# Performance work log

Hardware: AMD Instinct MI355X
Metric: run time of the kernel (lower is better)

## Reference

```python
import jax, jax.numpy as jnp
import numpy as np

N = 50000      # nodes
E = 800000     # edges (avg degree 16)
F_IN = 128
# (d_in, d_out) for the 9 GCNConv layers with width=256, n_layers=3
DIMS = [(128, 128), (128, 192), (192, 256), (256, 256), (256, 256), (256, 256), (256, 192), (192, 128), (128, 1)]
# ReLU after every conv except loop conv i==n_layers-2 (conv idx 4) and the final conv
RELU = [True, True, True, True, False, True, True, True, False]


def setup_inputs() -> dict:
    key = jax.random.key(0)
    ks = jax.random.split(key, 2 + 2 * len(DIMS))
    inp = {
        "x": jax.random.normal(ks[0], (N, F_IN), dtype=jnp.float32),
        "edge_index": jax.random.randint(ks[1], (2, E), 0, N, dtype=jnp.int64),
    }
    for i, (din, dout) in enumerate(DIMS):
        # Glorot-ish init for weights, small random bias (GCNConv has bias=True)
        inp[f"W{i}"] = jax.random.normal(ks[2 + 2 * i], (din, dout), dtype=jnp.float32) / np.float32(np.sqrt(din))
        inp[f"b{i}"] = jax.random.normal(ks[3 + 2 * i], (dout,), dtype=jnp.float32) * 0.01
    return inp


def _gcn_stack(x, src_f, dst_f, norm, Ws, bs):
    h = x
    for i in range(len(Ws)):
        h = h @ Ws[i]                                  # [N, dout] dense transform first (dout <= din mostly)
        msg = h[src_f] * norm[:, None]                 # gather + edge-normalize  [E+N, dout]
        h = jax.ops.segment_sum(msg, dst_f, num_segments=N) + bs[i]
        if RELU[i]:
            h = jax.nn.relu(h)
        # Dropout layers are identity in eval/inference mode.
    return h


def reference(x, edge_index,
              W0, b0, W1, b1, W2, b2, W3, b3, W4, b4, W5, b5, W6, b6, W7, b7, W8, b8):
    src, dst = edge_index[0], edge_index[1]
    loop = jnp.arange(N, dtype=src.dtype)
    # GCNConv default: add self loops, symmetric normalization D^{-1/2}(A+I)D^{-1/2}
    src_f = jnp.concatenate([src, loop])
    dst_f = jnp.concatenate([dst, loop])
    deg = jax.ops.segment_sum(jnp.ones(E + N, dtype=x.dtype), dst_f, num_segments=N)
    dinv = jax.lax.rsqrt(jnp.maximum(deg, 1.0))        # deg >= 1 thanks to self loops
    norm = dinv[src_f] * dinv[dst_f]                   # per-edge coefficient [E+N]
    Ws = [W0, W1, W2, W3, W4, W5, W6, W7, W8]
    bs = [b0, b1, b2, b3, b4, b5, b6, b7, b8]
    return _gcn_stack(x, src_f, dst_f, norm, Ws, bs)   # [N, 1]
```

## Files before the change

kernel.cpp:

```cpp
#include <hip/hip_runtime.h>


#define TPB 256

using bf16x8 = __attribute__((ext_vector_type(8))) __bf16;
using f32x4  = __attribute__((ext_vector_type(4))) float;
using f32x2  = __attribute__((ext_vector_type(2))) float;

__device__ __forceinline__ unsigned bf16rne(float x) {
    unsigned u = __float_as_uint(x);
    return (u + 0x7fffu + ((u >> 16) & 1u)) >> 16;
}

__device__ __forceinline__ void stage16(const unsigned short* g, unsigned short* l) {
#if __has_builtin(__builtin_amdgcn_global_load_lds)
    __builtin_amdgcn_global_load_lds((const __attribute__((address_space(1))) void*)g,
                                     (__attribute__((address_space(3))) void*)l, 16, 0, 0);
#else
    *(uint4*)((char*)l + (threadIdx.x & 63) * 16) = *(const uint4*)g;
#endif
}


__global__ void zinit_kernel(int* cnt, int* fill, unsigned* edges2, int n, int ecap) {
    int i = blockIdx.x * blockDim.x + threadIdx.x;
    if (i < n) { cnt[i] = 0; fill[i] = 0; }
    if (i < ecap) edges2[i] = 0u;
}

__global__ void count_kernel(const int* __restrict__ dst, int* __restrict__ cnt, int E) {
    int e = blockIdx.x * blockDim.x + threadIdx.x;
    if (e < E) atomicAdd(&cnt[dst[e]], 1);
}

__global__ void dinv_kernel(const int* __restrict__ cnt, float* __restrict__ dinv, int n) {
    int i = blockIdx.x * blockDim.x + threadIdx.x;
    if (i < n) dinv[i] = rsqrtf((float)(cnt[i] + 1));
}


__global__ void blockhist_kernel(const int* __restrict__ cnt, int* __restrict__ localRank,
                                 int* __restrict__ hb, int n, int nb) {
    __shared__ int h[64];
    int t = threadIdx.x;
    if (t < 64) h[t] = 0;
    __syncthreads();
    int i = blockIdx.x * TPB + t;
    if (i < n) {
        int d = cnt[i]; if (d > 63) d = 63;
        localRank[i] = atomicAdd(&h[d], 1);
    }
    __syncthreads();
    if (t < 64) hb[t * nb + blockIdx.x] = h[t];
}

__global__ __launch_bounds__(256) void sortscan_kernel(int* __restrict__ hb, int nb) {
    __shared__ int sh[64 * 256];
    __shared__ int tot[64], base[64];
    int t = threadIdx.x;
    int total = 64 * nb;
    for (int i = t; i < total; i += 256) sh[i] = hb[i];
    __syncthreads();
    if (t < 64) {
        int run = 0;
        for (int b = 0; b < nb; b++) {
            int v = sh[t * nb + b];
            sh[t * nb + b] = run;
            run += v;
        }
        tot[t] = run;
    }
    __syncthreads();
    if (t == 0) {
        int acc = 0;
        for (int b = 0; b < 64; b++) { base[b] = acc; acc += tot[b]; }
    }
    __syncthreads();
    for (int i = t; i < total; i += 256) hb[i] = sh[i] + base[i / nb];
}

__global__ void scatter2_kernel(const int* __restrict__ cnt,
                                const int* __restrict__ localRank, const int* __restrict__ hb,
                                int* __restrict__ perm, int* __restrict__ pcnt,
                                int* __restrict__ iperm, int n, int nb) {
    int i = blockIdx.x * TPB + threadIdx.x;
    if (i >= n) return;
    int c = cnt[i];
    int d = c; if (d > 63) d = 63;
    int pos = hb[d * nb + blockIdx.x] + localRank[i];
    perm[pos] = i;
    pcnt[pos] = c;
    iperm[i] = pos;
}

__global__ void scanpad_kernel(const int* __restrict__ pcnt, int* __restrict__ prowp2,
                               int* __restrict__ bsums, int n) {
    __shared__ int sh[TPB];
    int t = threadIdx.x;
    int i = blockIdx.x * TPB + t;
    int v = (i < n) ? ((pcnt[i] + 1 + 7) & ~7) : 0;
    sh[t] = v;
    __syncthreads();
    for (int off = 1; off < TPB; off <<= 1) {
        int x = (t >= off) ? sh[t - off] : 0;
        __syncthreads();
        sh[t] += x;
        __syncthreads();
    }
    if (i < n) prowp2[i] = sh[t] - v;
    if (t == TPB - 1) bsums[blockIdx.x] = sh[t];
}

__global__ void scan2_kernel(int* __restrict__ bsums, int nb) {
    __shared__ int sh[TPB];
    int t = threadIdx.x;
    int v = (t < nb) ? bsums[t] : 0;
    sh[t] = v;
    __syncthreads();
    for (int off = 1; off < TPB; off <<= 1) {
        int x = (t >= off) ? sh[t - off] : 0;
        __syncthreads();
        sh[t] += x;
        __syncthreads();
    }
    if (t < nb) bsums[t] = sh[t] - v;
}

__global__ void scan3_kernel(int* __restrict__ rowp, const int* __restrict__ bsums, int n) {
    int i = blockIdx.x * TPB + threadIdx.x;
    if (i < n) rowp[i] += bsums[blockIdx.x];
}

__global__ void fillself_kernel(const int* __restrict__ src, const int* __restrict__ dst,
                                const float* __restrict__ dinv,
                                const int* __restrict__ iperm, const int* __restrict__ prowp2,
                                int* __restrict__ fill, const int* __restrict__ cnt,
                                unsigned* __restrict__ edges2, int E, int n) {
    int id = blockIdx.x * blockDim.x + threadIdx.x;
    if (id < E) {
        int s = src[id], d = dst[id];
        int pos = prowp2[iperm[d]] + atomicAdd(&fill[d], 1);
        edges2[pos] = (unsigned)s | (bf16rne(dinv[s] * dinv[d]) << 16);
    } else if (id < E + n) {
        int i = id - E;
        float dv = dinv[i];
        edges2[prowp2[iperm[i]] + cnt[i]] = (unsigned)i | (bf16rne(dv * dv) << 16);
    }
}


struct WPtrs { const float* p[8]; };

__global__ void wt_all_kernel(WPtrs wp, unsigned short* __restrict__ Wts) {
    const int cum[9] = {0, 16384, 40960, 90112, 155648, 221184, 286720, 335872, 360448};
    const int Ns[8] = {128, 192, 256, 256, 256, 256, 192, 128};
    const int Ks[8] = {128, 128, 192, 256, 256, 256, 256, 192};
    int id = blockIdx.x * blockDim.x + threadIdx.x;
    if (id >= 360448) return;
    int L = 0;
#pragma unroll
    for (int t = 1; t < 8; t++) if (id >= cum[t]) L = t;
    int lid = id - cum[L];
    int N = Ns[L], K = Ks[L];
    int k = lid / N, n = lid - k * N;
    Wts[cum[L] + n * K + k] = (unsigned short)bf16rne(wp.p[L][lid]);
}

__global__ void cvt_bf16_kernel(const float* __restrict__ in, unsigned short* __restrict__ out,
                                int n4) {
    int i = blockIdx.x * blockDim.x + threadIdx.x;
    if (i >= n4) return;
    float4 v = ((const float4*)in)[i];
    uint2 o;
    o.x = bf16rne(v.x) | (bf16rne(v.y) << 16);
    o.y = bf16rne(v.z) | (bf16rne(v.w) << 16);
    ((uint2*)out)[i] = o;
}


__global__ __launch_bounds__(256) void gemm_mfma_kernel(
    const unsigned short* __restrict__ A, const unsigned short* __restrict__ Wt,
    const float* __restrict__ bias, unsigned short* __restrict__ C,
    int M, int K, int Nc, int doBias, int doRelu, int outChunked) {
    __shared__ unsigned short Qb[128 * 64];
    __shared__ unsigned short Pb[128 * 64];
    int tid = threadIdx.x;
    int l = tid & 63, w = tid >> 6;
    int node0 = blockIdx.x * 128, feat0 = blockIdx.y * 128;

    f32x4 acc[4][4];
#pragma unroll
    for (int i = 0; i < 4; i++)
#pragma unroll
        for (int j = 0; j < 4; j++) acc[i][j] = (f32x4){0.f, 0.f, 0.f, 0.f};

    const unsigned short* gQ[4];
    const unsigned short* gP[4];
    unsigned short* lQ[4];
    unsigned short* lP[4];
#pragma unroll
    for (int h = 0; h < 4; h++) {
        int slot = tid + h * 256;
        int r = slot >> 3, q = slot & 7;
        int qg = q ^ (r & 7);
        int nd = node0 + r; if (nd > M - 1) nd = M - 1;
        int ft = feat0 + r; if (ft > Nc - 1) ft = Nc - 1;
        gQ[h] = A + (size_t)nd * K + qg * 8;
        gP[h] = Wt + (size_t)ft * K + qg * 8;
        lQ[h] = Qb + (size_t)(w * 64 + h * 256) * 8;
        lP[h] = Pb + (size_t)(w * 64 + h * 256) * 8;
    }

    int q4 = l >> 4, m16 = l & 15;
    int featHalf = w & 1, nodeHalf = w >> 1;
    int rP0 = featHalf * 64 + m16;
    int rQ0 = nodeHalf * 64 + m16;
    int sw = m16 & 7;

    for (int k0 = 0; k0 < K; k0 += 64) {
        __syncthreads();
#pragma unroll
        for (int h = 0; h < 4; h++) {
            stage16(gQ[h] + k0, lQ[h]);
            stage16(gP[h] + k0, lP[h]);
        }
        __syncthreads();
#pragma unroll
        for (int ko = 0; ko < 2; ko++) {
            bf16x8 pf[4], qf[4];
#pragma unroll
            for (int i = 0; i < 4; i++)
                pf[i] = *(const bf16x8*)(Pb + (rP0 + i * 16) * 64 + ((ko * 4 + q4) ^ sw) * 8);
#pragma unroll
            for (int j = 0; j < 4; j++)
                qf[j] = *(const bf16x8*)(Qb + (rQ0 + j * 16) * 64 + ((ko * 4 + q4) ^ sw) * 8);
#pragma unroll
            for (int i = 0; i < 4; i++)
#pragma unroll
                for (int j = 0; j < 4; j++)
                    acc[i][j] = __builtin_amdgcn_mfma_f32_16x16x32_bf16(pf[i], qf[j],
                                                                        acc[i][j], 0, 0, 0);
        }
    }

#pragma unroll
    for (int i = 0; i < 4; i++) {
        int gf0 = feat0 + featHalf * 64 + i * 16 + q4 * 4;
        if (gf0 >= Nc) continue;
        float4 bv = make_float4(0.f, 0.f, 0.f, 0.f);
        if (doBias) bv = *(const float4*)(bias + gf0);
        size_t cb = outChunked ? ((size_t)(gf0 >> 5) * ((size_t)M * 32) + (gf0 & 31))
                               : (size_t)gf0;
#pragma unroll
        for (int j = 0; j < 4; j++) {
            int gn = node0 + nodeHalf * 64 + j * 16 + m16;
            if (gn >= M) continue;
            f32x4 v = acc[i][j];
            float x0 = v[0] + bv.x, x1 = v[1] + bv.y;
            float x2 = v[2] + bv.z, x3 = v[3] + bv.w;
            if (doRelu) {
                x0 = fmaxf(x0, 0.f); x1 = fmaxf(x1, 0.f);
                x2 = fmaxf(x2, 0.f); x3 = fmaxf(x3, 0.f);
            }
            uint2 o;
            o.x = bf16rne(x0) | (bf16rne(x1) << 16);
            o.y = bf16rne(x2) | (bf16rne(x3) << 16);
            size_t off = outChunked ? (cb + (size_t)gn * 32) : (cb + (size_t)gn * Nc);
            *(uint2*)(C + off) = o;
        }
    }
}

__global__ void gemv128_bf16_kernel(const unsigned short* __restrict__ A,
                                    const float* __restrict__ w,
                                    float* __restrict__ out, int M) {
    int wid = (blockIdx.x * blockDim.x + threadIdx.x) >> 6;
    int lane = threadIdx.x & 63;
    if (wid >= M) return;
    const unsigned short* a = A + (size_t)wid * 128;
    float a0 = __uint_as_float((unsigned)a[lane] << 16);
    float a1 = __uint_as_float((unsigned)a[lane + 64] << 16);
    float s = a0 * w[lane] + a1 * w[lane + 64];
#pragma unroll
    for (int off = 32; off > 0; off >>= 1) s += __shfl_down(s, off);
    if (lane == 0) out[wid] = s;
}


__global__ __launch_bounds__(256) void agg_group_kernel(
    const uint2* __restrict__ in, const int* __restrict__ prowp2,
    const int* __restrict__ pcnt, const int* __restrict__ perm,
    const unsigned* __restrict__ edges2,
    const float* __restrict__ bias, uint2* __restrict__ out,
    int Q, int upx, int ngPerUnit, int NG, int n_nodes, int rowVec2,
    int doBias, int doRelu, int outChunked) {
    int xcd = blockIdx.x & 7;
    int slot = blockIdx.x >> 3;
    int u = slot / ngPerUnit;
    int ngIdx = slot - u * ngPerUnit;
    int unit = xcd * upx + u;
    int chunk = unit / Q;
    int q = unit - chunk * Q;
    int ng = ngIdx * Q + q;
    if (ng >= NG) return;

    int wave = threadIdx.x >> 6;
    int lane = threadIdx.x & 63;
    int group = lane >> 3, fl = lane & 7;
    int i = ng * 32 + wave * 8 + group;
    if (i >= n_nodes) return;

    const uint2* sfl = in + (size_t)chunk * n_nodes * 8 + fl;
    int s0 = prowp2[i];
    int c = pcnt[i] + 1;
    int cpad = (c + 7) & ~7;
    int node = perm[i];
    const uint4* ep = (const uint4*)(edges2 + s0);

    f32x2 aA[4], aB[4];
#pragma unroll
    for (int k = 0; k < 4; k++) { aA[k] = (f32x2){0.f, 0.f}; aB[k] = (f32x2){0.f, 0.f}; }

    uint4 ea = ep[0], eb = ep[1];
    for (int base = 0; base < cpad; base += 8) {
        uint4 na = ep[2], nb = ep[3];
        ep += 2;
        unsigned e[8] = {ea.x, ea.y, ea.z, ea.w, eb.x, eb.y, eb.z, eb.w};
        uint2 p[8];
#pragma unroll
        for (int j = 0; j < 8; j++) p[j] = sfl[(size_t)(e[j] & 0xffffu) * 8];
#pragma unroll
        for (int j = 0; j < 8; j++) {
            float wgt = __uint_as_float(e[j] & 0xffff0000u);
            int k = j & 3;
            f32x2 v0 = {__uint_as_float(p[j].x << 16),
                        __uint_as_float(p[j].x & 0xffff0000u)};
            f32x2 v1 = {__uint_as_float(p[j].y << 16),
                        __uint_as_float(p[j].y & 0xffff0000u)};
            f32x2 w2 = {wgt, wgt};
            aA[k] += w2 * v0;
            aB[k] += w2 * v1;
        }
        ea = na; eb = nb;
    }
    f32x2 sA = (aA[0] + aA[1]) + (aA[2] + aA[3]);
    f32x2 sB = (aB[0] + aB[1]) + (aB[2] + aB[3]);

    if (doBias) {
        float4 bb = ((const float4*)bias)[chunk * 8 + fl];
        sA += (f32x2){bb.x, bb.y};
        sB += (f32x2){bb.z, bb.w};
    }
    if (doRelu) {
        sA[0] = fmaxf(sA[0], 0.f); sA[1] = fmaxf(sA[1], 0.f);
        sB[0] = fmaxf(sB[0], 0.f); sB[1] = fmaxf(sB[1], 0.f);
    }
    uint2 o;
    o.x = bf16rne(sA[0]) | (bf16rne(sA[1]) << 16);
    o.y = bf16rne(sB[0]) | (bf16rne(sB[1]) << 16);
    size_t oi = outChunked ? ((size_t)chunk * n_nodes * 8 + (size_t)node * 8 + fl)
                           : ((size_t)node * rowVec2 + chunk * 8 + fl);
    out[oi] = o;
}

__global__ void agg1_kernel(const float* __restrict__ in, const int* __restrict__ prowp2,
                            const int* __restrict__ pcnt, const int* __restrict__ perm,
                            const unsigned* __restrict__ edges2,
                            const float* __restrict__ bias, float* __restrict__ out,
                            int n_nodes) {
    int n = blockIdx.x * blockDim.x + threadIdx.x;
    if (n >= n_nodes) return;
    float acc = 0.f;
    int s0 = prowp2[n];
    int c = pcnt[n] + 1;
    for (int j = 0; j < c; j++) {
        unsigned e = edges2[s0 + j];
        acc += __uint_as_float(e & 0xffff0000u) * in[e & 0xffffu];
    }
    acc += bias[0];
    out[perm[n]] = acc;
}


extern "C" void kernel_launch(void* const* d_in, const int* in_sizes, int n_in,
                              void* d_out, int out_size, void* d_ws, size_t ws_size,
                              hipStream_t stream) {
    const float* x = (const float*)d_in[0];
    const int* ei = (const int*)d_in[1];
    const int Nn = in_sizes[0] / 128;
    const int E = in_sizes[1] / 2;
    const int* src = ei;
    const int* dst = ei + E;
    const int ecap = E + 8 * Nn + 64;

    char* ws = (char*)d_ws;
    size_t off = 0;
    auto alloc = [&](size_t bytes) -> char* {
        char* p = ws + off;
        off = (off + bytes + 255) & ~(size_t)255;
        return p;
    };
    int* cnt = (int*)alloc((size_t)Nn * 4);
    int* fill = (int*)alloc((size_t)Nn * 4);
    int* bsums = (int*)alloc(1024);
    float* dinv = (float*)alloc((size_t)Nn * 4);
    int* localRank = (int*)alloc((size_t)Nn * 4);
    int* hb = (int*)alloc((size_t)64 * 256 * 4);
    int* perm = (int*)alloc((size_t)Nn * 4);
    int* pcnt = (int*)alloc((size_t)Nn * 4);
    int* iperm = (int*)alloc((size_t)Nn * 4);
    int* prowp2 = (int*)alloc((size_t)Nn * 4);
    unsigned* edges2 = (unsigned*)alloc((size_t)ecap * 4);
    unsigned short* T = (unsigned short*)alloc((size_t)Nn * 256 * 2);
    unsigned short* H = (unsigned short*)alloc((size_t)Nn * 256 * 2);
    unsigned short* Bx = (unsigned short*)alloc((size_t)Nn * 128 * 2);
    float* F = (float*)alloc((size_t)Nn * 4);
    unsigned short* Wts = (unsigned short*)alloc((size_t)400000 * 2);
    (void)ws_size;

    const int dims[9][2] = {{128,128},{128,192},{192,256},{256,256},{256,256},
                            {256,256},{256,192},{192,128},{128,1}};
    unsigned short* Wt[8];
    {
        size_t o = 0;
        for (int i = 0; i < 8; i++) { Wt[i] = Wts + o; o += (size_t)dims[i][0] * dims[i][1]; }
    }

    int nbN = (Nn + TPB - 1) / TPB;
    int nbE = (E + TPB - 1) / TPB;
    int nbEN = (E + Nn + TPB - 1) / TPB;
    int nbC = (ecap + TPB - 1) / TPB;

    zinit_kernel<<<nbC, TPB, 0, stream>>>(cnt, fill, edges2, Nn, ecap);
    count_kernel<<<nbE, TPB, 0, stream>>>(dst, cnt, E);
    dinv_kernel<<<nbN, TPB, 0, stream>>>(cnt, dinv, Nn);
    blockhist_kernel<<<nbN, TPB, 0, stream>>>(cnt, localRank, hb, Nn, nbN);
    sortscan_kernel<<<1, 256, 0, stream>>>(hb, nbN);
    scatter2_kernel<<<nbN, TPB, 0, stream>>>(cnt, localRank, hb, perm, pcnt, iperm,
                                             Nn, nbN);
    scanpad_kernel<<<nbN, TPB, 0, stream>>>(pcnt, prowp2, bsums, Nn);
    scan2_kernel<<<1, TPB, 0, stream>>>(bsums, nbN);
    scan3_kernel<<<nbN, TPB, 0, stream>>>(prowp2, bsums, Nn);
    fillself_kernel<<<nbEN, TPB, 0, stream>>>(src, dst, dinv, iperm, prowp2, fill, cnt,
                                              edges2, E, Nn);

    WPtrs wp;
    for (int i = 0; i < 8; i++) wp.p[i] = (const float*)d_in[2 + 2 * i];
    wt_all_kernel<<<(360448 + TPB - 1) / TPB, TPB, 0, stream>>>(wp, Wts);
    cvt_bf16_kernel<<<(Nn * 32 + TPB - 1) / TPB, TPB, 0, stream>>>(x, Bx, Nn * 32);

    auto gemm = [&](const unsigned short* A, int i, unsigned short* C, int K, int Nc,
                    int doBias, int doRelu, int outChunked) {
        const float* b = (const float*)d_in[3 + 2 * i];
        dim3 grid((Nn + 127) / 128, (Nc + 127) / 128);
        gemm_mfma_kernel<<<grid, 256, 0, stream>>>(A, Wt[i], b, C, Nn, K, Nc,
                                                   doBias, doRelu, outChunked);
    };
    int NG = (Nn + 31) / 32;
    auto agg = [&](const unsigned short* inb, unsigned short* outb, int w, int i,
                   int doBias, int doRelu, int outChunked) {
        int nch = w / 32;
        int Q = (nch == 8) ? 1 : (nch == 6) ? 4 : 2;
        int upx = nch * Q / 8;
        int ngPerUnit = (NG + Q - 1) / Q;
        int blocksPerXcd = upx * ngPerUnit;
        const float* b = (const float*)d_in[3 + 2 * i];
        agg_group_kernel<<<blocksPerXcd * 8, 256, 0, stream>>>(
            (const uint2*)inb, prowp2, pcnt, perm, edges2, b, (uint2*)outb,
            Q, upx, ngPerUnit, NG, Nn, w / 4, doBias, doRelu, outChunked);
    };

    gemm(Bx, 0, T, 128, 128, 0, 0, 1);
    agg(T, H, 128, 0, 1, 1, 1);
    agg(H, T, 128, 1, 0, 0, 0);
    gemm(T, 1, H, 128, 192, 1, 1, 1);
    agg(H, T, 192, 2, 0, 0, 0);
    gemm(T, 2, H, 192, 256, 1, 1, 0);
    gemm(H, 3, T, 256, 256, 0, 0, 1);
    agg(T, H, 256, 3, 1, 1, 0);
    gemm(H, 4, T, 256, 256, 0, 0, 1);
    agg(T, H, 256, 4, 1, 0, 0);
    gemm(H, 5, T, 256, 256, 0, 0, 1);
    agg(T, H, 256, 5, 1, 1, 0);
    gemm(H, 6, T, 256, 192, 0, 0, 1);
    agg(T, H, 192, 6, 1, 1, 0);
    gemm(H, 7, T, 192, 128, 0, 0, 1);
    agg(T, H, 128, 7, 1, 1, 0);
    gemv128_bf16_kernel<<<(Nn + 3) / 4, 256, 0, stream>>>(H, (const float*)d_in[2 + 16],
                                                          F, Nn);
    agg1_kernel<<<nbN, TPB, 0, stream>>>(F, prowp2, pcnt, perm, edges2,
                                         (const float*)d_in[3 + 16], (float*)d_out, Nn);
}
```

Measured before the change: 685.4 us.

## Drop padded CSR rows and share edge words across lanes by shuffle

Removes the padding of each CSR row to a multiple of 8, so the edge array no longer needs zero-initialising over its padded capacity. In the aggregation kernel, each 8-lane group now loads one edge word per lane, guarded by the row length, and broadcasts them with __shfl instead of every lane reading two uint4 per step. Separately, the dinv computation is folded into the blockhist kernel, saving one launch. The cost is eight shuffles per batch of 8 edges; padded slots read edge 0 with weight 0, which is harmless.

```diff
diff --git a/kernel.cpp b/kernel.cpp
--- a/kernel.cpp
+++ b/kernel.cpp
@@ -22,10 +22,9 @@
 }
 
 
-__global__ void zinit_kernel(int* cnt, int* fill, unsigned* edges2, int n, int ecap) {
+__global__ void zinit_kernel(int* cnt, int* fill, int n) {
     int i = blockIdx.x * blockDim.x + threadIdx.x;
     if (i < n) { cnt[i] = 0; fill[i] = 0; }
-    if (i < ecap) edges2[i] = 0u;
 }
 
 __global__ void count_kernel(const int* __restrict__ dst, int* __restrict__ cnt, int E) {
@@ -33,21 +32,19 @@
     if (e < E) atomicAdd(&cnt[dst[e]], 1);
 }
 
-__global__ void dinv_kernel(const int* __restrict__ cnt, float* __restrict__ dinv, int n) {
-    int i = blockIdx.x * blockDim.x + threadIdx.x;
-    if (i < n) dinv[i] = rsqrtf((float)(cnt[i] + 1));
-}
-
 
 __global__ void blockhist_kernel(const int* __restrict__ cnt, int* __restrict__ localRank,
-                                 int* __restrict__ hb, int n, int nb) {
+                                 int* __restrict__ hb, float* __restrict__ dinv,
+                                 int n, int nb) {
     __shared__ int h[64];
     int t = threadIdx.x;
     if (t < 64) h[t] = 0;
     __syncthreads();
     int i = blockIdx.x * TPB + t;
     if (i < n) {
-        int d = cnt[i]; if (d > 63) d = 63;
+        int c = cnt[i];
+        dinv[i] = rsqrtf((float)(c + 1));
+        int d = c; if (d > 63) d = 63;
         localRank[i] = atomicAdd(&h[d], 1);
     }
     __syncthreads();
@@ -93,12 +90,12 @@
     iperm[i] = pos;
 }
 
-__global__ void scanpad_kernel(const int* __restrict__ pcnt, int* __restrict__ prowp2,
-                               int* __restrict__ bsums, int n) {
+__global__ void scan1_kernel(const int* __restrict__ pcnt, int* __restrict__ prowp2,
+                             int* __restrict__ bsums, int n) {
     __shared__ int sh[TPB];
     int t = threadIdx.x;
     int i = blockIdx.x * TPB + t;
-    int v = (i < n) ? ((pcnt[i] + 1 + 7) & ~7) : 0;
+    int v = (i < n) ? (pcnt[i] + 1) : 0;
     sh[t] = v;
     __syncthreads();
     for (int off = 1; off < TPB; off <<= 1) {
@@ -307,28 +304,29 @@
     int wave = threadIdx.x >> 6;
     int lane = threadIdx.x & 63;
     int group = lane >> 3, fl = lane & 7;
+    int gb = lane & ~7;
     int i = ng * 32 + wave * 8 + group;
     if (i >= n_nodes) return;
 
-    const uint2* sfl = in + (size_t)chunk * n_nodes * 8 + fl;
+    const uint2* slice = in + (size_t)chunk * n_nodes * 8;
     int s0 = prowp2[i];
     int c = pcnt[i] + 1;
-    int cpad = (c + 7) & ~7;
     int node = perm[i];
-    const uint4* ep = (const uint4*)(edges2 + s0);
 
     f32x2 aA[4], aB[4];
 #pragma unroll
     for (int k = 0; k < 4; k++) { aA[k] = (f32x2){0.f, 0.f}; aB[k] = (f32x2){0.f, 0.f}; }
 
-    uint4 ea = ep[0], eb = ep[1];
-    for (int base = 0; base < cpad; base += 8) {
-        uint4 na = ep[2], nb = ep[3];
-        ep += 2;
-        unsigned e[8] = {ea.x, ea.y, ea.z, ea.w, eb.x, eb.y, eb.z, eb.w};
+    unsigned ew = (fl < c) ? edges2[s0 + fl] : 0u;
+    for (int base = 0; base < c; base += 8) {
+        int nidx = base + 8 + fl;
+        unsigned ewn = (nidx < c) ? edges2[s0 + nidx] : 0u;
+        unsigned e[8];
+#pragma unroll
+        for (int j = 0; j < 8; j++) e[j] = (unsigned)__shfl((int)ew, gb + j);
         uint2 p[8];
 #pragma unroll
-        for (int j = 0; j < 8; j++) p[j] = sfl[(size_t)(e[j] & 0xffffu) * 8];
+        for (int j = 0; j < 8; j++) p[j] = slice[(int)(e[j] & 0xffffu) * 8 + fl];
 #pragma unroll
         for (int j = 0; j < 8; j++) {
             float wgt = __uint_as_float(e[j] & 0xffff0000u);
@@ -341,7 +339,7 @@
             aA[k] += w2 * v0;
             aB[k] += w2 * v1;
         }
-        ea = na; eb = nb;
+        ew = ewn;
     }
     f32x2 sA = (aA[0] + aA[1]) + (aA[2] + aA[3]);
     f32x2 sB = (aB[0] + aB[1]) + (aB[2] + aB[3]);
@@ -391,7 +389,6 @@
     const int E = in_sizes[1] / 2;
     const int* src = ei;
     const int* dst = ei + E;
-    const int ecap = E + 8 * Nn + 64;
 
     char* ws = (char*)d_ws;
     size_t off = 0;
@@ -410,7 +407,7 @@
     int* pcnt = (int*)alloc((size_t)Nn * 4);
     int* iperm = (int*)alloc((size_t)Nn * 4);
     int* prowp2 = (int*)alloc((size_t)Nn * 4);
-    unsigned* edges2 = (unsigned*)alloc((size_t)ecap * 4);
+    unsigned* edges2 = (unsigned*)alloc((size_t)(E + Nn + 64) * 4);
     unsigned short* T = (unsigned short*)alloc((size_t)Nn * 256 * 2);
     unsigned short* H = (unsigned short*)alloc((size_t)Nn * 256 * 2);
     unsigned short* Bx = (unsigned short*)alloc((size_t)Nn * 128 * 2);
@@ -429,16 +426,14 @@
     int nbN = (Nn + TPB - 1) / TPB;
     int nbE = (E + TPB - 1) / TPB;
     int nbEN = (E + Nn + TPB - 1) / TPB;
-    int nbC = (ecap + TPB - 1) / TPB;
-
-    zinit_kernel<<<nbC, TPB, 0, stream>>>(cnt, fill, edges2, Nn, ecap);
+
+    zinit_kernel<<<nbN, TPB, 0, stream>>>(cnt, fill, Nn);
     count_kernel<<<nbE, TPB, 0, stream>>>(dst, cnt, E);
-    dinv_kernel<<<nbN, TPB, 0, stream>>>(cnt, dinv, Nn);
-    blockhist_kernel<<<nbN, TPB, 0, stream>>>(cnt, localRank, hb, Nn, nbN);
+    blockhist_kernel<<<nbN, TPB, 0, stream>>>(cnt, localRank, hb, dinv, Nn, nbN);
     sortscan_kernel<<<1, 256, 0, stream>>>(hb, nbN);
     scatter2_kernel<<<nbN, TPB, 0, stream>>>(cnt, localRank, hb, perm, pcnt, iperm,
                                              Nn, nbN);
-    scanpad_kernel<<<nbN, TPB, 0, stream>>>(pcnt, prowp2, bsums, Nn);
+    scan1_kernel<<<nbN, TPB, 0, stream>>>(pcnt, prowp2, bsums, Nn);
     scan2_kernel<<<1, TPB, 0, stream>>>(bsums, nbN);
     scan3_kernel<<<nbN, TPB, 0, stream>>>(prowp2, bsums, Nn);
     fillself_kernel<<<nbEN, TPB, 0, stream>>>(src, dst, dinv, iperm, prowp2, fill, cnt,
```

After: 659.0 us. 1.04x faster.
